# Performance work log

Hardware: AMD Instinct MI355X
Metric: run time of the kernel (lower is better)

Reference implementation:

```python
import jax, jax.numpy as jnp
import numpy as np

COST_BBOX = 1.0
COST_GIOU = 1.0
TOPK = 5


def _make_boxes(key, b, n):
    # valid xyxy boxes in [0,1]: centers + small positive sizes
    kc, ks = jax.random.split(key)
    cxy = jax.random.uniform(kc, (b, n, 2))
    wh = jax.random.uniform(ks, (b, n, 2)) * 0.2 + 0.01
    return jnp.concatenate([cxy - wh / 2, cxy + wh / 2], axis=-1)


def setup_inputs() -> dict:
    key = jax.random.key(0)
    k1, k2, k3, k4 = jax.random.split(key, 4)
    B, NP, NG = 8, 5000, 300
    return {
        "pred_box": _make_boxes(k1, B, NP),
        "pred_obj": jax.random.normal(k3, (B, NP), dtype=jnp.float32),
        "gt_box": _make_boxes(k2, B, NG),
        "gt_obj": jax.random.normal(k4, (B, NG), dtype=jnp.float32),
    }


def pairwise_giou(pb, gb):
    # pb: [B,N,4], gb: [B,M,4] in xyxy -> giou [B,N,M]
    area_p = (pb[..., 2] - pb[..., 0]) * (pb[..., 3] - pb[..., 1])  # [B,N]
    area_g = (gb[..., 2] - gb[..., 0]) * (gb[..., 3] - gb[..., 1])  # [B,M]
    lt = jnp.maximum(pb[:, :, None, :2], gb[:, None, :, :2])  # [B,N,M,2]
    rb = jnp.minimum(pb[:, :, None, 2:], gb[:, None, :, 2:])
    wh = jnp.clip(rb - lt, 0.0)
    inter = wh[..., 0] * wh[..., 1]                                  # [B,N,M]
    union = area_p[:, :, None] + area_g[:, None, :] - inter
    iou = inter / union
    # smallest enclosing box
    lt_e = jnp.minimum(pb[:, :, None, :2], gb[:, None, :, :2])
    rb_e = jnp.maximum(pb[:, :, None, 2:], gb[:, None, :, 2:])
    wh_e = jnp.clip(rb_e - lt_e, 0.0)
    area_e = wh_e[..., 0] * wh_e[..., 1]
    return iou - (area_e - union) / area_e


def cost_matrix(pred_box, gt_box):
    # L1 cdist: [B,N,M]
    cost_bbox = jnp.sum(jnp.abs(pred_box[:, :, None, :] - gt_box[:, None, :, :]), axis=-1)
    cost_giou = 1.0 - pairwise_giou(pred_box, gt_box)
    return COST_BBOX * cost_bbox + COST_GIOU * cost_giou


def reference(pred_box, pred_obj, gt_box, gt_obj):
    C = cost_matrix(pred_box, gt_box)            # [B, N_pred, N_gt]
    Ct = jnp.swapaxes(C, 1, 2)                   # [B, N_gt, N_pred]
    _, idx = jax.lax.top_k(-Ct, TOPK)            # smallest-cost preds per gt: [B, N_gt, TOPK]
    B, M, _ = idx.shape
    matched_pred = idx.reshape(B, M * TOPK).astype(jnp.int32)
    matched_gt = jnp.broadcast_to(jnp.repeat(jnp.arange(M, dtype=jnp.int32), TOPK)[None, :], (B, M * TOPK))
    return matched_pred, matched_gt
```

## Files before the change

kernel.cpp:

```cpp
#include <hip/hip_runtime.h>

#pragma clang fp contract(off)

typedef unsigned long long u64;
typedef float f4 __attribute__((ext_vector_type(4)));

#define TOPK 5
#define WAVES 4

#define CE(x, y) do { const u64 _a = (x), _b = (y); const bool _l = _b < _a; \
                      (x) = _l ? _b : _a; (y) = _l ? _a : _b; } while (0)

__device__ __forceinline__ float fast_div(float a, float b) {
    float r = __builtin_amdgcn_rcpf(b);
    r = fmaf(fmaf(-b, r, 1.0f), r, r);
    float q = a * r;
    q = fmaf(fmaf(-b, q, a), r, q);
    return q;
}

__device__ __forceinline__ u64 eval_key(const f4 pb, const f4 gb,
                                        const float g_area, const int p) {
    const float area_p = (pb.z - pb.x) * (pb.w - pb.y);
    const float cost_bbox = fabsf(pb.x - gb.x) + fabsf(pb.y - gb.y)
                          + fabsf(pb.z - gb.z) + fabsf(pb.w - gb.w);
    const float ltx = fmaxf(pb.x, gb.x), lty = fmaxf(pb.y, gb.y);
    const float rbx = fminf(pb.z, gb.z), rby = fminf(pb.w, gb.w);
    const float iw = fmaxf(rbx - ltx, 0.0f), ih = fmaxf(rby - lty, 0.0f);
    const float inter = iw * ih;
    const float uni = area_p + g_area - inter;
    const float iou = fast_div(inter, uni);
    const float ex1 = fminf(pb.x, gb.x), ey1 = fminf(pb.y, gb.y);
    const float ex2 = fmaxf(pb.z, gb.z), ey2 = fmaxf(pb.w, gb.w);
    const float area_e = (ex2 - ex1) * (ey2 - ey1);
    const float giou = iou - fast_div(area_e - uni, area_e);
    const float cost = cost_bbox + (1.0f - giou);
    return ((u64)__float_as_uint(cost) << 32) | (unsigned)p;
}

__global__ __launch_bounds__(64 * WAVES) void matcher_topk_kernel(
    const float* __restrict__ pred_box,
    const float* __restrict__ gt_box,
    int* __restrict__ out_pred,
    int* __restrict__ out_gt,
    int B, int NP, int NG)
{
    const int pairsPerB = (NG + 1) >> 1;
    const int tp = blockIdx.x;
    const int b  = tp / pairsPerB;
    const int j  = tp - b * pairsPerB;
    const int m0 = 2 * j;
    const bool has1 = (m0 + 1 < NG);

    const int wid  = threadIdx.x >> 6;
    const int lane = threadIdx.x & 63;
    const int myGt = wid >> 1;
    const int half = wid & 1;

    const f4 gb = ((const f4*)gt_box)[b * NG + (myGt ? (has1 ? m0 + 1 : m0) : m0)];
    const float g_area = (gb.z - gb.x) * (gb.w - gb.y);

    const int NPm1  = NP - 1;
    const int hN    = (NP + 1) >> 1;
    const int start = half ? hN : 0;
    const int pend  = half ? NP : hN;

    u64 k0 = ~0ULL, k1 = ~0ULL, k2 = ~0ULL, k3 = ~0ULL, k4 = ~0ULL;

    const f4* pbase = (const f4*)pred_box + (size_t)b * NP;

#define GLOADF(g, rA, rB, rC, rD) do {                                          \
    const f4* _p = pbase + (start + ((g) << 8) + lane);                         \
    asm volatile("global_load_dwordx4 %0, %1, off"             : "=v"(rA) : "v"(_p)); \
    asm volatile("global_load_dwordx4 %0, %1, off offset:1024" : "=v"(rB) : "v"(_p)); \
    asm volatile("global_load_dwordx4 %0, %1, off offset:2048" : "=v"(rC) : "v"(_p)); \
    asm volatile("global_load_dwordx4 %0, %1, off offset:3072" : "=v"(rD) : "v"(_p)); \
} while (0)

#define GLOADS(g, rA, rB, rC, rD) do {                                          \
    const int _i = start + ((g) << 8) + lane;                                   \
    const f4* _p0 = pbase + min(_i,       NPm1);                                \
    const f4* _p1 = pbase + min(_i + 64,  NPm1);                                \
    const f4* _p2 = pbase + min(_i + 128, NPm1);                                \
    const f4* _p3 = pbase + min(_i + 192, NPm1);                                \
    asm volatile("global_load_dwordx4 %0, %1, off" : "=v"(rA) : "v"(_p0));      \
    asm volatile("global_load_dwordx4 %0, %1, off" : "=v"(rB) : "v"(_p1));      \
    asm volatile("global_load_dwordx4 %0, %1, off" : "=v"(rC) : "v"(_p2));      \
    asm volatile("global_load_dwordx4 %0, %1, off" : "=v"(rD) : "v"(_p3));      \
} while (0)

#define W(n) do {                                         \
    asm volatile("s_waitcnt vmcnt(" #n ")");              \
    __builtin_amdgcn_sched_barrier(0);                    \
} while (0)

#define PROCG(g, TAIL, rA, rB, rC, rD) do {                                  \
    const int _i0 = start + ((g) << 8) + lane;                               \
    u64 kA = eval_key(rA, gb, g_area, _i0);                                  \
    u64 kB = eval_key(rB, gb, g_area, _i0 + 64);                             \
    u64 kC = eval_key(rC, gb, g_area, _i0 + 128);                            \
    u64 kD = eval_key(rD, gb, g_area, _i0 + 192);                            \
    if (TAIL) {                                                              \
        kA = (_i0       < pend) ? kA : ~0ULL;                                \
        kB = (_i0 + 64  < pend) ? kB : ~0ULL;                                \
        kC = (_i0 + 128 < pend) ? kC : ~0ULL;                                \
        kD = (_i0 + 192 < pend) ? kD : ~0ULL;                                \
    }                                                                        \
    CE(kA, kB); CE(kC, kD); CE(kA, kC); CE(kB, kD); CE(kB, kC);              \
    u64 n0 = k0;                                                             \
    u64 n1 = k1 < kD ? k1 : kD;                                              \
    u64 n2 = k2 < kC ? k2 : kC;                                              \
    u64 n3 = k3 < kB ? k3 : kB;                                              \
    u64 n4 = k4 < kA ? k4 : kA;                                              \
    CE(n0, n1); CE(n3, n4); CE(n2, n4); CE(n2, n3); CE(n1, n4);              \
    CE(n0, n3); CE(n0, n2); CE(n1, n3); CE(n1, n2);                          \
    k0 = n0; k1 = n1; k2 = n2; k3 = n3; k4 = n4;                             \
} while (0)

    f4 xA, xB, xC, xD;
    f4 yA, yB, yC, yD;
    f4 zA, zB, zC, zD;
    f4 uA, uB, uC, uD;

    GLOADF(0, xA, xB, xC, xD);
    GLOADF(1, yA, yB, yC, yD);
    GLOADF(2, zA, zB, zC, zD);
    GLOADF(3, uA, uB, uC, uD);

    W(8);
    PROCG(0, false, xA, xB, xC, xD);
    PROCG(1, false, yA, yB, yC, yD);
    GLOADF(4, xA, xB, xC, xD);
    GLOADF(5, yA, yB, yC, yD);
    W(8);
    PROCG(2, false, zA, zB, zC, zD);
    PROCG(3, false, uA, uB, uC, uD);
    GLOADF(6, zA, zB, zC, zD);
    GLOADF(7, uA, uB, uC, uD);
    W(8);
    PROCG(4, false, xA, xB, xC, xD);
    PROCG(5, false, yA, yB, yC, yD);
    GLOADF(8, xA, xB, xC, xD);
    GLOADS(9, yA, yB, yC, yD);
    W(8);
    PROCG(6, false, zA, zB, zC, zD);
    PROCG(7, false, uA, uB, uC, uD);
    W(0);
    PROCG(8, false, xA, xB, xC, xD);
    PROCG(9, true,  yA, yB, yC, yD);

#undef GLOADF
#undef GLOADS
#undef W
#undef PROCG

    #pragma unroll
    for (int off = 1; off < 64; off <<= 1) {
        const u64 b0 = __shfl_xor(k0, off);
        const u64 b1 = __shfl_xor(k1, off);
        const u64 b2 = __shfl_xor(k2, off);
        const u64 b3 = __shfl_xor(k3, off);
        const u64 b4 = __shfl_xor(k4, off);
        u64 m0_ = k0 < b4 ? k0 : b4;
        u64 m1_ = k1 < b3 ? k1 : b3;
        u64 m2_ = k2 < b2 ? k2 : b2;
        u64 m3_ = k3 < b1 ? k3 : b1;
        u64 m4_ = k4 < b0 ? k4 : b0;
        CE(m0_, m1_); CE(m3_, m4_); CE(m2_, m4_); CE(m2_, m3_); CE(m1_, m4_);
        CE(m0_, m3_); CE(m0_, m2_); CE(m1_, m3_); CE(m1_, m2_);
        k0 = m0_; k1 = m1_; k2 = m2_; k3 = m3_; k4 = m4_;
    }

    __shared__ u64 lds[WAVES][TOPK];
    if (lane == 0) {
        lds[wid][0] = k0; lds[wid][1] = k1; lds[wid][2] = k2;
        lds[wid][3] = k3; lds[wid][4] = k4;
    }
    __syncthreads();

    if (threadIdx.x < 2) {
        const int which = threadIdx.x;
        if (which == 0 || has1) {
            const int mm = m0 + which;
            int h0 = 0, h1 = 0;
            const int base = (b * NG + mm) * TOPK;
            #pragma unroll
            for (int r = 0; r < TOPK; ++r) {
                const u64 v0 = lds[which * 2][h0];
                const u64 v1 = lds[which * 2 + 1][h1];
                const bool t = v0 < v1;
                const u64 best = t ? v0 : v1;
                h0 += t; h1 += !t;
                out_pred[base + r] = (int)(unsigned)(best & 0xFFFFFFFFu);
                out_gt[base + r]   = mm;
            }
        }
    }
}

extern "C" void kernel_launch(void* const* d_in, const int* in_sizes, int n_in,
                              void* d_out, int out_size, void* d_ws, size_t ws_size,
                              hipStream_t stream) {
    const float* pred_box = (const float*)d_in[0];
    const float* gt_box   = (const float*)d_in[2];

    const int NP = 5000;
    const int B  = in_sizes[1] / NP;
    const int NG = in_sizes[3] / B;

    int* out_pred = (int*)d_out;
    int* out_gt   = out_pred + B * NG * TOPK;

    const int pairsPerB = (NG + 1) >> 1;
    const int blocks = B * pairsPerB;
    hipLaunchKernelGGL(matcher_topk_kernel, dim3(blocks), dim3(64 * WAVES), 0, stream,
                       pred_box, gt_box, out_pred, out_gt, B, NP, NG);
}
```

Before: 34.76 us.

## Prune candidates via L1 lower bound against wave-wide fifth-best threshold

After three groups are processed, the per-wave top-5 is reduced across lanes to get a threshold cost. The cheap L1 box distance is a lower bound on the total cost, so the remaining groups compute it first. The expensive GIoU evaluation and insertion run only when some lane passes the bound. This trades the sorting network for per-element wave-uniform branches and a scalar insertion into the per-lane top-5.

```diff
diff --git a/kernel.cpp b/kernel.cpp
--- a/kernel.cpp
+++ b/kernel.cpp
@@ -10,6 +10,20 @@
 
 #define CE(x, y) do { const u64 _a = (x), _b = (y); const bool _l = _b < _a; \
                       (x) = _l ? _b : _a; (y) = _l ? _a : _b; } while (0)
+
+#define INSERT(nk) do {                            \
+    const u64 _n = (nk);                           \
+    const bool l0 = _n < k0;                       \
+    const bool l1 = _n < k1;                       \
+    const bool l2 = _n < k2;                       \
+    const bool l3 = _n < k3;                       \
+    const bool l4 = _n < k4;                       \
+    k4 = l4 ? (l3 ? k3 : _n) : k4;                 \
+    k3 = l3 ? (l2 ? k2 : _n) : k3;                 \
+    k2 = l2 ? (l1 ? k1 : _n) : k2;                 \
+    k1 = l1 ? (l0 ? k0 : _n) : k1;                 \
+    k0 = l0 ? _n : k0;                             \
+} while (0)
 
 __device__ __forceinline__ float fast_div(float a, float b) {
     float r = __builtin_amdgcn_rcpf(b);
@@ -19,11 +33,10 @@
     return q;
 }
 
-__device__ __forceinline__ u64 eval_key(const f4 pb, const f4 gb,
-                                        const float g_area, const int p) {
+__device__ __forceinline__ u64 eval_rest(const f4 pb, const float cb,
+                                         const f4 gb, const float g_area,
+                                         const int p) {
     const float area_p = (pb.z - pb.x) * (pb.w - pb.y);
-    const float cost_bbox = fabsf(pb.x - gb.x) + fabsf(pb.y - gb.y)
-                          + fabsf(pb.z - gb.z) + fabsf(pb.w - gb.w);
     const float ltx = fmaxf(pb.x, gb.x), lty = fmaxf(pb.y, gb.y);
     const float rbx = fminf(pb.z, gb.z), rby = fminf(pb.w, gb.w);
     const float iw = fmaxf(rbx - ltx, 0.0f), ih = fmaxf(rby - lty, 0.0f);
@@ -34,8 +47,13 @@
     const float ex2 = fmaxf(pb.z, gb.z), ey2 = fmaxf(pb.w, gb.w);
     const float area_e = (ex2 - ex1) * (ey2 - ey1);
     const float giou = iou - fast_div(area_e - uni, area_e);
-    const float cost = cost_bbox + (1.0f - giou);
+    const float cost = cb + (1.0f - giou);
     return ((u64)__float_as_uint(cost) << 32) | (unsigned)p;
+}
+
+__device__ __forceinline__ float bbox_l1(const f4 pb, const f4 gb) {
+    return fabsf(pb.x - gb.x) + fabsf(pb.y - gb.y)
+         + fabsf(pb.z - gb.z) + fabsf(pb.w - gb.w);
 }
 
 __global__ __launch_bounds__(64 * WAVES) void matcher_topk_kernel(
@@ -94,18 +112,12 @@
     __builtin_amdgcn_sched_barrier(0);                    \
 } while (0)
 
-#define PROCG(g, TAIL, rA, rB, rC, rD) do {                                  \
+#define PROCG(g, rA, rB, rC, rD) do {                                        \
     const int _i0 = start + ((g) << 8) + lane;                               \
-    u64 kA = eval_key(rA, gb, g_area, _i0);                                  \
-    u64 kB = eval_key(rB, gb, g_area, _i0 + 64);                             \
-    u64 kC = eval_key(rC, gb, g_area, _i0 + 128);                            \
-    u64 kD = eval_key(rD, gb, g_area, _i0 + 192);                            \
-    if (TAIL) {                                                              \
-        kA = (_i0       < pend) ? kA : ~0ULL;                                \
-        kB = (_i0 + 64  < pend) ? kB : ~0ULL;                                \
-        kC = (_i0 + 128 < pend) ? kC : ~0ULL;                                \
-        kD = (_i0 + 192 < pend) ? kD : ~0ULL;                                \
-    }                                                                        \
+    u64 kA = eval_rest(rA, bbox_l1(rA, gb), gb, g_area, _i0);                \
+    u64 kB = eval_rest(rB, bbox_l1(rB, gb), gb, g_area, _i0 + 64);           \
+    u64 kC = eval_rest(rC, bbox_l1(rC, gb), gb, g_area, _i0 + 128);          \
+    u64 kD = eval_rest(rD, bbox_l1(rD, gb), gb, g_area, _i0 + 192);          \
     CE(kA, kB); CE(kC, kD); CE(kA, kC); CE(kB, kD); CE(kB, kC);              \
     u64 n0 = k0;                                                             \
     u64 n1 = k1 < kD ? k1 : kD;                                              \
@@ -117,6 +129,25 @@
     k0 = n0; k1 = n1; k2 = n2; k3 = n3; k4 = n4;                             \
 } while (0)
 
+#define PROCS(pb_, idx_, TAIL) do {                                          \
+    const float _cb = bbox_l1(pb_, gb);                                      \
+    bool _pass = (__float_as_uint(_cb) <= thr_bits);                         \
+    if (TAIL) _pass = _pass && ((idx_) < pend);                              \
+    if (__any((int)_pass)) {                                                 \
+        u64 _k = eval_rest(pb_, _cb, gb, g_area, (idx_));                    \
+        if (TAIL) _k = ((idx_) < pend) ? _k : ~0ULL;                         \
+        INSERT(_k);                                                          \
+    }                                                                        \
+} while (0)
+
+#define PROCSG(g, TAIL, rA, rB, rC, rD) do {                                 \
+    const int _i0 = start + ((g) << 8) + lane;                               \
+    PROCS(rA, _i0,       TAIL);                                              \
+    PROCS(rB, _i0 + 64,  TAIL);                                              \
+    PROCS(rC, _i0 + 128, TAIL);                                              \
+    PROCS(rD, _i0 + 192, TAIL);                                              \
+} while (0)
+
     f4 xA, xB, xC, xD;
     f4 yA, yB, yC, yD;
     f4 zA, zB, zC, zD;
@@ -127,32 +158,60 @@
     GLOADF(2, zA, zB, zC, zD);
     GLOADF(3, uA, uB, uC, uD);
 
-    W(8);
-    PROCG(0, false, xA, xB, xC, xD);
-    PROCG(1, false, yA, yB, yC, yD);
+    unsigned thr_bits = 0xFFFFFFFFu;
+
+    W(8);
+    PROCG(0, xA, xB, xC, xD);
+    PROCG(1, yA, yB, yC, yD);
     GLOADF(4, xA, xB, xC, xD);
     GLOADF(5, yA, yB, yC, yD);
-    W(8);
-    PROCG(2, false, zA, zB, zC, zD);
-    PROCG(3, false, uA, uB, uC, uD);
+
+    W(8);
+    PROCG(2, zA, zB, zC, zD);
+    {
+        u64 c0 = k0, c1 = k1, c2 = k2, c3 = k3, c4 = k4;
+        #pragma unroll
+        for (int off = 1; off < 64; off <<= 1) {
+            const u64 b0 = __shfl_xor(c0, off);
+            const u64 b1 = __shfl_xor(c1, off);
+            const u64 b2 = __shfl_xor(c2, off);
+            const u64 b3 = __shfl_xor(c3, off);
+            const u64 b4 = __shfl_xor(c4, off);
+            u64 m0_ = c0 < b4 ? c0 : b4;
+            u64 m1_ = c1 < b3 ? c1 : b3;
+            u64 m2_ = c2 < b2 ? c2 : b2;
+            u64 m3_ = c3 < b1 ? c3 : b1;
+            u64 m4_ = c4 < b0 ? c4 : b0;
+            CE(m0_, m1_); CE(m3_, m4_); CE(m2_, m4_); CE(m2_, m3_); CE(m1_, m4_);
+            CE(m0_, m3_); CE(m0_, m2_); CE(m1_, m3_); CE(m1_, m2_);
+            c0 = m0_; c1 = m1_; c2 = m2_; c3 = m3_; c4 = m4_;
+        }
+        thr_bits = __builtin_amdgcn_readfirstlane((unsigned)(c4 >> 32));
+    }
+    PROCSG(3, false, uA, uB, uC, uD);
     GLOADF(6, zA, zB, zC, zD);
     GLOADF(7, uA, uB, uC, uD);
-    W(8);
-    PROCG(4, false, xA, xB, xC, xD);
-    PROCG(5, false, yA, yB, yC, yD);
+
+    W(8);
+    PROCSG(4, false, xA, xB, xC, xD);
+    PROCSG(5, false, yA, yB, yC, yD);
     GLOADF(8, xA, xB, xC, xD);
     GLOADS(9, yA, yB, yC, yD);
-    W(8);
-    PROCG(6, false, zA, zB, zC, zD);
-    PROCG(7, false, uA, uB, uC, uD);
+
+    W(8);
+    PROCSG(6, false, zA, zB, zC, zD);
+    PROCSG(7, false, uA, uB, uC, uD);
+
     W(0);
-    PROCG(8, false, xA, xB, xC, xD);
-    PROCG(9, true,  yA, yB, yC, yD);
+    PROCSG(8, false, xA, xB, xC, xD);
+    PROCSG(9, true,  yA, yB, yC, yD);
 
 #undef GLOADF
 #undef GLOADS
 #undef W
 #undef PROCG
+#undef PROCS
+#undef PROCSG
 
     #pragma unroll
     for (int off = 1; off < 64; off <<= 1) {
```

Measured after the change: 39.49 us. 1.14x slower.
